# Kernel optimization log

Hardware: AMD Instinct MI355X
Metric: run time of the kernel (lower is better)

## Reference

```python
import jax, jax.numpy as jnp
import numpy as np

T, N, D, H, L = 256, 128, 1024, 1024, 2  # seq len, batch, input, hidden, layers


def setup_inputs() -> dict:
    key = jax.random.key(0)
    ks = jax.random.split(key, 7)
    s = 1.0 / np.sqrt(H)  # PyTorch LSTMCell init: U(-1/sqrt(H), 1/sqrt(H))
    return {
        "x": jax.random.normal(ks[0], (T, N, D), jnp.float32),
        "h0": jax.random.normal(ks[1], (L, N, H), jnp.float32),
        "c0": jax.random.normal(ks[2], (L, N, H), jnp.float32),
        # stacked per-layer params (layer 0 input dim == H so shapes match)
        "W_ih": jax.random.uniform(ks[3], (L, 4 * H, D), jnp.float32, -s, s),
        "W_hh": jax.random.uniform(ks[4], (L, 4 * H, H), jnp.float32, -s, s),
        "b_ih": jax.random.uniform(ks[5], (L, 4 * H), jnp.float32, -s, s),
        "b_hh": jax.random.uniform(ks[6], (L, 4 * H), jnp.float32, -s, s),
    }


def _lstm_cell(x, h, c, Wih, Whh, b):
    # gates layout (PyTorch order): input, forget, cell(g), output
    gates = x @ Wih.T + h @ Whh.T + b  # [N, 4H]
    i, f, g, o = jnp.split(gates, 4, axis=-1)
    c_new = jax.nn.sigmoid(f) * c + jax.nn.sigmoid(i) * jnp.tanh(g)
    h_new = jax.nn.sigmoid(o) * jnp.tanh(c_new)
    return h_new, c_new


def reference(x, h0, c0, W_ih, W_hh, b_ih, b_hh):
    num_layers = h0.shape[0]
    b = b_ih + b_hh  # [L, 4H]

    def step(carry, x_t):
        h, c = carry  # each [L, N, H]
        inp = x_t
        hs, cs = [], []
        for l in range(num_layers):  # small fixed layer count
            h_l, c_l = _lstm_cell(inp, h[l], c[l], W_ih[l], W_hh[l], b[l])
            hs.append(h_l)
            cs.append(c_l)
            inp = h_l  # mirrors x[t] = h[i] feeding the next layer
        return (jnp.stack(hs), jnp.stack(cs)), None

    (h, c), _ = jax.lax.scan(step, (h0, c0), x)
    return h[-1]  # [N, H] last layer hidden at final timestep
```

## Files before the change

kernel.cpp:

```cpp
#include <hip/hip_runtime.h>


typedef _Float16 f16;
typedef f16  v8f16 __attribute__((ext_vector_type(8)));
typedef float v4f32 __attribute__((ext_vector_type(4)));

#define TSTEPS 256
#define SLOT   131072u
static constexpr size_t HS_BANK = (size_t)258 * SLOT;

#define SZ_W     ((size_t)2*4096*2048*2)
#define SZ_B     ((size_t)2*4096*4)
#define SZ_HSEQ  ((size_t)2*258*SLOT*2)
#define SZ_BAR   ((size_t)8192)
#define SZ_XF    ((size_t)256*128*1024*2)
#define NEED1    (SZ_W + SZ_B + SZ_HSEQ + SZ_BAR)
#define NEED2    (NEED1 + SZ_XF)

__global__ void lstm_init(const float* __restrict__ x,
                          const float* __restrict__ h0,
                          const float* __restrict__ Wih, const float* __restrict__ Whh,
                          const float* __restrict__ bih, const float* __restrict__ bhh,
                          f16* __restrict__ wsW, float* __restrict__ wsB,
                          f16* __restrict__ hseq, unsigned* __restrict__ bar,
                          f16* __restrict__ xf, int do_xf)
{
    size_t tid  = (size_t)blockIdx.x * blockDim.x + threadIdx.x;
    size_t nthr = (size_t)gridDim.x * blockDim.x;
    for (size_t i = tid; i < 16777216u; i += nthr) {
        unsigned l = (unsigned)(i >> 23), rem = (unsigned)(i & 8388607u);
        unsigned col = rem >> 11, k = rem & 2047u;
        float v = (k < 1024u) ? Wih[(size_t)l*4194304u + (size_t)col*1024u + k]
                              : Whh[(size_t)l*4194304u + (size_t)col*1024u + (k-1024u)];
        wsW[i] = (f16)v;
    }
    for (size_t i = tid; i < 8192u; i += nthr) wsB[i] = bih[i] + bhh[i];
    for (size_t i = tid; i < 131072u; i += nthr) {
        unsigned n = (unsigned)(i >> 10), k = (unsigned)(i & 1023u);
        unsigned dst = ((k >> 3) << 10) + (n << 3) + (k & 7u);
        hseq[dst]           = (f16)h0[i];
        hseq[HS_BANK + dst] = (f16)h0[131072u + i];
    }
    for (size_t i = tid; i < 2048u; i += nthr) bar[i] = 0u;
    if (do_xf) {
        for (size_t i = tid; i < 33554432u; i += nthr) xf[i] = (f16)x[i];
    }
}

__device__ __forceinline__ float sigmoid_fast(float v) { return 1.0f / (1.0f + __expf(-v)); }
__device__ __forceinline__ float tanh_fast(float v)    { return 1.0f - 2.0f / (__expf(2.0f*v) + 1.0f); }

__device__ __forceinline__ v8f16 cvt8(v4f32 lo, v4f32 hi) {
    v8f16 r;
    r[0]=(f16)lo[0]; r[1]=(f16)lo[1]; r[2]=(f16)lo[2]; r[3]=(f16)lo[3];
    r[4]=(f16)hi[0]; r[5]=(f16)hi[1]; r[6]=(f16)hi[2]; r[7]=(f16)hi[3];
    return r;
}

__device__ __forceinline__ unsigned ld_cnt(const unsigned* p) {
    return __hip_atomic_load(p, __ATOMIC_RELAXED, __HIP_MEMORY_SCOPE_AGENT);
}

#define CHUNK 8

__device__ __forceinline__ void load_row(const f16* p, int off,
                                         v8f16 a0[CHUNK], v8f16 a1[CHUNK])
{
    #pragma unroll
    for (int i = 0; i < CHUNK; ++i) {
        a0[i] = *(const v8f16*)(p + off + 32*i);
        a1[i] = *(const v8f16*)(p + off + 16384 + 32*i);
    }
}

__device__ __forceinline__ void load_sm(const f16* p, int off,
                                        v8f16 a0[CHUNK], v8f16 a1[CHUNK])
{
    #pragma unroll
    for (int i = 0; i < CHUNK; ++i) {
        a0[i] = *(const v8f16*)(p + off + 4096*i);
        a1[i] = *(const v8f16*)(p + off + 128 + 4096*i);
    }
}

__device__ __forceinline__ void mfma_chunk(const v8f16 a0[CHUNK], const v8f16 a1[CHUNK],
                                           const f16 (*wl)[2056], int l15, int kq, int kbase,
                                           v4f32 acc[2][2])
{
    #pragma unroll
    for (int i = 0; i < CHUNK; ++i) {
        int k = kbase + 32*i;
        v8f16 b0 = *(const v8f16*)(&wl[l15     ][k + kq]);
        v8f16 b1 = *(const v8f16*)(&wl[16 + l15][k + kq]);
        acc[0][0] = __builtin_amdgcn_mfma_f32_16x16x32_f16(a0[i], b0, acc[0][0], 0, 0, 0);
        acc[0][1] = __builtin_amdgcn_mfma_f32_16x16x32_f16(a0[i], b1, acc[0][1], 0, 0, 0);
        acc[1][0] = __builtin_amdgcn_mfma_f32_16x16x32_f16(a1[i], b0, acc[1][0], 0, 0, 0);
        acc[1][1] = __builtin_amdgcn_mfma_f32_16x16x32_f16(a1[i], b1, acc[1][1], 0, 0, 0);
    }
}

__device__ __forceinline__ void reduce_splits(v4f32 acc[2][2], float (*gl)[36],
                                              int rb, int quad, int l15, int ks)
{
    if (ks == 0) {
        #pragma unroll
        for (int mt = 0; mt < 2; ++mt) {
            int rrow = (rb << 5) + (mt << 4) + (quad << 2);
            #pragma unroll
            for (int r = 0; r < 4; ++r) {
                gl[rrow + r][l15     ] = acc[mt][0][r];
                gl[rrow + r][16 + l15] = acc[mt][1][r];
            }
        }
    }
    __syncthreads();
    if (ks == 1) {
        #pragma unroll
        for (int mt = 0; mt < 2; ++mt) {
            int rrow = (rb << 5) + (mt << 4) + (quad << 2);
            #pragma unroll
            for (int r = 0; r < 4; ++r) {
                gl[rrow + r][l15     ] += acc[mt][0][r];
                gl[rrow + r][16 + l15] += acc[mt][1][r];
            }
        }
    }
    __syncthreads();
}

__device__ __forceinline__ void cell2(const float (*gl)[36], int n1, int u,
                                      float bi, float bf, float bg, float bo,
                                      float& cr0, float& cr1, float& h0o, float& h1o)
{
    {
        float gi = gl[n1][u]      + bi;
        float gf = gl[n1][8 + u]  + bf;
        float gg = gl[n1][16 + u] + bg;
        float go = gl[n1][24 + u] + bo;
        float cn = sigmoid_fast(gf) * cr0 + sigmoid_fast(gi) * tanh_fast(gg);
        cr0 = cn;
        h0o = sigmoid_fast(go) * tanh_fast(cn);
    }
    {
        int n = n1 + 64;
        float gi = gl[n][u]      + bi;
        float gf = gl[n][8 + u]  + bf;
        float gg = gl[n][16 + u] + bg;
        float go = gl[n][24 + u] + bo;
        float cn = sigmoid_fast(gf) * cr1 + sigmoid_fast(gi) * tanh_fast(gg);
        cr1 = cn;
        h1o = sigmoid_fast(go) * tanh_fast(cn);
    }
}

__device__ __forceinline__ void store_h_slot(f16 (*hst)[8], f16* slotbase, int s,
                                             int tid, int n1, int u,
                                             float hv0, float hv1)
{
    hst[n1     ][u] = (f16)hv0;
    hst[n1 + 64][u] = (f16)hv1;
    __syncthreads();
    if (tid < 128) {
        union { v8f16 v; unsigned long long q[2]; } c;
        c.v = *(const v8f16*)&hst[tid][0];
        unsigned long long* gp = (unsigned long long*)(slotbase + ((size_t)s << 10) + (tid << 3));
        __hip_atomic_store(gp,     c.q[0], __ATOMIC_RELAXED, __HIP_MEMORY_SCOPE_AGENT);
        __hip_atomic_store(gp + 1, c.q[1], __ATOMIC_RELAXED, __HIP_MEMORY_SCOPE_AGENT);
    }
}

template<bool XF16>
__global__ void __launch_bounds__(512)
lstm_main(const float* __restrict__ x, const f16* __restrict__ xf,
          const f16* __restrict__ wsW, const float* __restrict__ wsB,
          f16* __restrict__ hseq, const float* __restrict__ c0,
          float* __restrict__ out, unsigned* __restrict__ bar)
{
    __shared__ f16   wlds[32][2056];
    __shared__ float glds[128][36];
    __shared__ f16   hst[128][8];

    const int tid   = threadIdx.x;
    const int bid   = blockIdx.x;
    const int xcd   = bid & 7;
    const int layer = (xcd >> 2);
    const int s     = (bid >> 3) * 4 + (xcd & 3);
    const int lane  = tid & 63;
    const int wave  = tid >> 6;
    const int quad  = lane >> 4;
    const int l15   = lane & 15;
    const int rb    = wave & 3;
    const int ks    = wave >> 2;

    for (int idx = tid; idx < 8192; idx += 512) {
        int cc = idx >> 8;
        int k8 = (idx & 255) << 3;
        int col = ((cc >> 3) << 10) + (s << 3) + (cc & 7);
        *(v8f16*)(&wlds[cc][k8]) =
            *(const v8f16*)(wsW + (((size_t)(layer*4096 + col)) << 11) + k8);
    }

    const int u  = tid & 7;
    const int jg = (s << 3) + u;
    const float bi = wsB[layer*4096 +        jg];
    const float bf = wsB[layer*4096 + 1024 + jg];
    const float bg = wsB[layer*4096 + 2048 + jg];
    const float bo = wsB[layer*4096 + 3072 + jg];
    const int n1 = tid >> 3;
    float cr0 = c0[((size_t)layer << 17) + ((size_t)n1 << 10) + jg];
    float cr1 = c0[((size_t)layer << 17) + ((size_t)(n1 + 64) << 10) + jg];

    __syncthreads();

    const int kq   = quad << 3;
    const int row0 = (rb << 5) + l15;
    const int kslc = ks << 9;
    const int arow = (row0 << 10) + kslc + kq;
    const int jrow = (((kslc + kq) >> 3) << 10) + (row0 << 3);

    f16* h0b = hseq;
    f16* h1b = hseq + HS_BANK;
    unsigned* f0a = bar;
    unsigned* f0b = bar + 512;
    unsigned* f1  = bar + 1024;

    v8f16 A0[CHUNK], A1[CHUNK], C0[CHUNK], C1[CHUNK];

    if (layer == 0) {
        for (int t = 0; t < TSTEPS; ++t) {
            v4f32 acc[2][2] = {};

            if (XF16) {
                const f16* xp = xf + ((size_t)t << 17) + arow;
                load_row(xp, 0,   A0, A1);
                load_row(xp, 256, C0, C1);
                __builtin_amdgcn_sched_barrier(0);
                mfma_chunk(A0, A1, wlds, l15, kq, kslc,       acc);
                mfma_chunk(C0, C1, wlds, l15, kq, kslc + 256, acc);
            } else {
                const float* p0 = x + ((size_t)t << 17) + arow;
                const float* p1 = p0 + (16 << 10);
                #pragma unroll
                for (int k = 0; k < 512; k += 32) {
                    v4f32 w0 = *(const v4f32*)(p0 + k), w1 = *(const v4f32*)(p0 + k + 4);
                    v4f32 y0 = *(const v4f32*)(p1 + k), y1 = *(const v4f32*)(p1 + k + 4);
                    v8f16 a0 = cvt8(w0, w1);
                    v8f16 a1 = cvt8(y0, y1);
                    v8f16 b0 = *(const v8f16*)(&wlds[l15     ][kslc + k + kq]);
                    v8f16 b1 = *(const v8f16*)(&wlds[16 + l15][kslc + k + kq]);
                    acc[0][0] = __builtin_amdgcn_mfma_f32_16x16x32_f16(a0, b0, acc[0][0], 0, 0, 0);
                    acc[0][1] = __builtin_amdgcn_mfma_f32_16x16x32_f16(a0, b1, acc[0][1], 0, 0, 0);
                    acc[1][0] = __builtin_amdgcn_mfma_f32_16x16x32_f16(a1, b0, acc[1][0], 0, 0, 0);
                    acc[1][1] = __builtin_amdgcn_mfma_f32_16x16x32_f16(a1, b1, acc[1][1], 0, 0, 0);
                }
            }

            if (t > 0) {
                if (tid < 128) {
                    const unsigned* fp = f0a + (tid << 2);
                    unsigned need = (unsigned)t;
                    while (ld_cnt(fp) < need) __builtin_amdgcn_s_sleep(1);
                }
                __syncthreads();
            }

            {
                const f16* hp = h0b + (size_t)t * SLOT + jrow;
                load_sm(hp, 0,     A0, A1);
                load_sm(hp, 32768, C0, C1);
                __builtin_amdgcn_sched_barrier(0);
                mfma_chunk(A0, A1, wlds, l15, kq, 1024 + kslc,       acc);
                mfma_chunk(C0, C1, wlds, l15, kq, 1024 + kslc + 256, acc);
            }

            reduce_splits(acc, glds, rb, quad, l15, ks);

            float hv0, hv1;
            cell2(glds, n1, u, bi, bf, bg, bo, cr0, cr1, hv0, hv1);
            store_h_slot(hst, h0b + (size_t)(t + 1) * SLOT, s, tid, n1, u, hv0, hv1);

            __syncthreads();
            if (tid == 0) {
                __hip_atomic_store(f0a + (s << 2), (unsigned)(t + 1),
                                   __ATOMIC_RELAXED, __HIP_MEMORY_SCOPE_AGENT);
                __hip_atomic_store(f0b + (s << 2), (unsigned)(t + 1),
                                   __ATOMIC_RELAXED, __HIP_MEMORY_SCOPE_AGENT);
            }
        }
    } else {
        v8f16 D0[CHUNK], D1[CHUNK];
        for (int t = 0; t < TSTEPS; ++t) {
            {
                if (tid < 128) {
                    const unsigned* fp = f0b + (tid << 2);
                    unsigned need = (unsigned)(t + 1);
                    while (ld_cnt(fp) < need) __builtin_amdgcn_s_sleep(2);
                }
                __syncthreads();
            }

            v4f32 acc[2][2] = {};
            const f16* qp = h0b + (size_t)(t + 1) * SLOT + jrow;
            const f16* pp = h1b + (size_t)t * SLOT + jrow;

            load_sm(qp, 0,     A0, A1);
            load_sm(qp, 32768, C0, C1);
            __builtin_amdgcn_sched_barrier(0);

            if (t > 0) {
                if (tid < 128) {
                    const unsigned* fp = f1 + (tid << 2);
                    unsigned need = (unsigned)t;
                    while (ld_cnt(fp) < need) __builtin_amdgcn_s_sleep(2);
                }
            }
            __syncthreads();

            load_sm(pp, 0, D0, D1);
            __builtin_amdgcn_sched_barrier(0);
            mfma_chunk(A0, A1, wlds, l15, kq, kslc,       acc);
            load_sm(pp, 32768, A0, A1);
            __builtin_amdgcn_sched_barrier(0);
            mfma_chunk(C0, C1, wlds, l15, kq, kslc + 256, acc);
            mfma_chunk(D0, D1, wlds, l15, kq, 1024 + kslc,       acc);
            mfma_chunk(A0, A1, wlds, l15, kq, 1024 + kslc + 256, acc);

            reduce_splits(acc, glds, rb, quad, l15, ks);

            float hv0, hv1;
            cell2(glds, n1, u, bi, bf, bg, bo, cr0, cr1, hv0, hv1);
            if (t < TSTEPS - 1) {
                store_h_slot(hst, h1b + (size_t)(t + 1) * SLOT, s, tid, n1, u, hv0, hv1);
                __syncthreads();
                if (tid == 0)
                    __hip_atomic_store(f1 + (s << 2), (unsigned)(t + 1),
                                       __ATOMIC_RELAXED, __HIP_MEMORY_SCOPE_AGENT);
            } else {
                out[(n1 << 10) + jg] = hv0;
                out[((n1 + 64) << 10) + jg] = hv1;
            }
        }
    }
}

extern "C" void kernel_launch(void* const* d_in, const int* in_sizes, int n_in,
                              void* d_out, int out_size, void* d_ws, size_t ws_size,
                              hipStream_t stream) {
    const float* x   = (const float*)d_in[0];
    const float* h0  = (const float*)d_in[1];
    const float* c0  = (const float*)d_in[2];
    const float* Wih = (const float*)d_in[3];
    const float* Whh = (const float*)d_in[4];
    const float* bih = (const float*)d_in[5];
    const float* bhh = (const float*)d_in[6];
    float* out = (float*)d_out;

    char* ws = (char*)d_ws;
    const bool xf16 = (ws_size >= NEED2);

    f16*      wsW  = (f16*)ws;
    float*    wsB  = (float*)(ws + SZ_W);
    f16*      hseq = (f16*)(ws + SZ_W + SZ_B);
    unsigned* bar  = (unsigned*)(ws + SZ_W + SZ_B + SZ_HSEQ);
    f16*      xf   = (f16*)(ws + NEED1);
    int do_xf = xf16 ? 1 : 0;

    lstm_init<<<2048, 256, 0, stream>>>(x, h0, Wih, Whh, bih, bhh,
                                        wsW, wsB, hseq, bar, xf, do_xf);

    void* kargs[] = { (void*)&x, (void*)&xf, (void*)&wsW, (void*)&wsB,
                      (void*)&hseq, (void*)&c0, (void*)&out, (void*)&bar };
    if (xf16) {
        hipLaunchCooperativeKernel((void*)&lstm_main<true>, dim3(256), dim3(512), kargs, 0, stream);
    } else {
        hipLaunchCooperativeKernel((void*)&lstm_main<false>, dim3(256), dim3(512), kargs, 0, stream);
    }
}
```

Baseline: 3.139 ms.

## Precompute layer-0 input projections for all timesteps in a parallel prologue

Adds a prologue in which all 256 blocks (both layer groups, using layer-0 weights) compute x_t @ W_ih0^T for every timestep and write the gate preactivations to a workspace buffer in fp32 or fp16. A grid-wide flag barrier follows, then layer-1 blocks reload their own weights. The recurrent layer-0 loop then only does the h @ W_hh part and adds a prefetched gx vector, which shortens the serial critical path. This costs an extra large workspace buffer plus its memory traffic and a global barrier. Which variant runs depends on how much workspace is available.

After: 3.631 ms. 1.16x slower.

```diff
diff --git a/kernel.cpp b/kernel.cpp
--- a/kernel.cpp
+++ b/kernel.cpp
@@ -12,10 +12,14 @@
 #define SZ_W     ((size_t)2*4096*2048*2)
 #define SZ_B     ((size_t)2*4096*4)
 #define SZ_HSEQ  ((size_t)2*258*SLOT*2)
-#define SZ_BAR   ((size_t)8192)
+#define SZ_BAR   ((size_t)16384)
 #define SZ_XF    ((size_t)256*128*1024*2)
 #define NEED1    (SZ_W + SZ_B + SZ_HSEQ + SZ_BAR)
 #define NEED2    (NEED1 + SZ_XF)
+#define SZ_GX32  ((size_t)256*128*4096*4)
+#define SZ_GX16  ((size_t)256*128*4096*2)
+#define NEED3_32 (NEED2 + SZ_GX32)
+#define NEED3_16 (NEED2 + SZ_GX16)
 
 __global__ void lstm_init(const float* __restrict__ x,
                           const float* __restrict__ h0,
@@ -41,7 +45,7 @@
         hseq[dst]           = (f16)h0[i];
         hseq[HS_BANK + dst] = (f16)h0[131072u + i];
     }
-    for (size_t i = tid; i < 2048u; i += nthr) bar[i] = 0u;
+    for (size_t i = tid; i < 4096u; i += nthr) bar[i] = 0u;
     if (do_xf) {
         for (size_t i = tid; i < 33554432u; i += nthr) xf[i] = (f16)x[i];
     }
@@ -129,24 +133,25 @@
 }
 
 __device__ __forceinline__ void cell2(const float (*gl)[36], int n1, int u,
+                                      const float* gxv,
                                       float bi, float bf, float bg, float bo,
                                       float& cr0, float& cr1, float& h0o, float& h1o)
 {
     {
-        float gi = gl[n1][u]      + bi;
-        float gf = gl[n1][8 + u]  + bf;
-        float gg = gl[n1][16 + u] + bg;
-        float go = gl[n1][24 + u] + bo;
+        float gi = gl[n1][u]      + gxv[0] + bi;
+        float gf = gl[n1][8 + u]  + gxv[1] + bf;
+        float gg = gl[n1][16 + u] + gxv[2] + bg;
+        float go = gl[n1][24 + u] + gxv[3] + bo;
         float cn = sigmoid_fast(gf) * cr0 + sigmoid_fast(gi) * tanh_fast(gg);
         cr0 = cn;
         h0o = sigmoid_fast(go) * tanh_fast(cn);
     }
     {
         int n = n1 + 64;
-        float gi = gl[n][u]      + bi;
-        float gf = gl[n][8 + u]  + bf;
-        float gg = gl[n][16 + u] + bg;
-        float go = gl[n][24 + u] + bo;
+        float gi = gl[n][u]      + gxv[4] + bi;
+        float gf = gl[n][8 + u]  + gxv[5] + bf;
+        float gg = gl[n][16 + u] + gxv[6] + bg;
+        float go = gl[n][24 + u] + gxv[7] + bo;
         float cn = sigmoid_fast(gf) * cr1 + sigmoid_fast(gi) * tanh_fast(gg);
         cr1 = cn;
         h1o = sigmoid_fast(go) * tanh_fast(cn);
@@ -169,12 +174,41 @@
     }
 }
 
-template<bool XF16>
+__device__ __forceinline__ void stage_w(f16 (*wl)[2056], const f16* wsW,
+                                        int lyr, int s, int tid)
+{
+    for (int idx = tid; idx < 8192; idx += 512) {
+        int cc = idx >> 8;
+        int k8 = (idx & 255) << 3;
+        int col = ((cc >> 3) << 10) + (s << 3) + (cc & 7);
+        *(v8f16*)(&wl[cc][k8]) =
+            *(const v8f16*)(wsW + (((size_t)(lyr*4096 + col)) << 11) + k8);
+    }
+}
+
+template<int MODE>
+__device__ __forceinline__ void load_gx(const void* gxws, int t, int s, int tid, float gxv[8])
+{
+    size_t ge = (((size_t)t << 7) + (size_t)s) * 4096u + ((size_t)tid << 3);
+    if constexpr (MODE == 2) {
+        const v4f32* gp = (const v4f32*)((const float*)gxws + ge);
+        v4f32 ga = gp[0], gb = gp[1];
+        gxv[0]=ga[0]; gxv[1]=ga[1]; gxv[2]=ga[2]; gxv[3]=ga[3];
+        gxv[4]=gb[0]; gxv[5]=gb[1]; gxv[6]=gb[2]; gxv[7]=gb[3];
+    } else {
+        v8f16 gv = *(const v8f16*)((const f16*)gxws + ge);
+        #pragma unroll
+        for (int i = 0; i < 8; ++i) gxv[i] = (float)gv[i];
+    }
+}
+
+template<int MODE, bool XF16>
 __global__ void __launch_bounds__(512)
 lstm_main(const float* __restrict__ x, const f16* __restrict__ xf,
           const f16* __restrict__ wsW, const float* __restrict__ wsB,
           f16* __restrict__ hseq, const float* __restrict__ c0,
-          float* __restrict__ out, unsigned* __restrict__ bar)
+          float* __restrict__ out, unsigned* __restrict__ bar,
+          void* gxws)
 {
     __shared__ f16   wlds[32][2056];
     __shared__ float glds[128][36];
@@ -192,13 +226,7 @@
     const int rb    = wave & 3;
     const int ks    = wave >> 2;
 
-    for (int idx = tid; idx < 8192; idx += 512) {
-        int cc = idx >> 8;
-        int k8 = (idx & 255) << 3;
-        int col = ((cc >> 3) << 10) + (s << 3) + (cc & 7);
-        *(v8f16*)(&wlds[cc][k8]) =
-            *(const v8f16*)(wsW + (((size_t)(layer*4096 + col)) << 11) + k8);
-    }
+    stage_w(wlds, wsW, (MODE >= 1 && layer == 1) ? 0 : layer, s, tid);
 
     const int u  = tid & 7;
     const int jg = (s << 3) + u;
@@ -220,38 +248,94 @@
 
     f16* h0b = hseq;
     f16* h1b = hseq + HS_BANK;
-    unsigned* f0a = bar;
-    unsigned* f0b = bar + 512;
-    unsigned* f1  = bar + 1024;
+    unsigned* f0a  = bar;
+    unsigned* f0b  = bar + 512;
+    unsigned* f1   = bar + 1024;
+    unsigned* prep = bar + 1536;
 
     v8f16 A0[CHUNK], A1[CHUNK], C0[CHUNK], C1[CHUNK];
+    float gz[8] = {0,0,0,0,0,0,0,0};
+
+    if constexpr (MODE >= 1) {
+        const int tbase = (layer == 0) ? 0 : 128;
+        for (int tt = 0; tt < 128; ++tt) {
+            const int t = tbase + tt;
+            v4f32 acc[2][2] = {};
+            const f16* xp = xf + ((size_t)t << 17) + arow;
+            load_row(xp, 0,   A0, A1);
+            load_row(xp, 256, C0, C1);
+            __builtin_amdgcn_sched_barrier(0);
+            mfma_chunk(A0, A1, wlds, l15, kq, kslc,       acc);
+            mfma_chunk(C0, C1, wlds, l15, kq, kslc + 256, acc);
+            reduce_splits(acc, glds, rb, quad, l15, ks);
+            float g0 = glds[n1][u],      g1 = glds[n1][8+u];
+            float g2 = glds[n1][16+u],   g3 = glds[n1][24+u];
+            float g4 = glds[n1+64][u],   g5 = glds[n1+64][8+u];
+            float g6 = glds[n1+64][16+u],g7 = glds[n1+64][24+u];
+            __syncthreads();
+            size_t ge = (((size_t)t << 7) + (size_t)s) * 4096u + ((size_t)tid << 3);
+            if constexpr (MODE == 2) {
+                union { float f[8]; unsigned long long q[4]; } gu;
+                gu.f[0]=g0; gu.f[1]=g1; gu.f[2]=g2; gu.f[3]=g3;
+                gu.f[4]=g4; gu.f[5]=g5; gu.f[6]=g6; gu.f[7]=g7;
+                unsigned long long* gp = (unsigned long long*)((float*)gxws + ge);
+                #pragma unroll
+                for (int i = 0; i < 4; ++i)
+                    __hip_atomic_store(gp + i, gu.q[i],
+                                       __ATOMIC_RELAXED, __HIP_MEMORY_SCOPE_AGENT);
+            } else {
+                union { f16 h[8]; unsigned long long q[2]; } gh;
+                gh.h[0]=(f16)g0; gh.h[1]=(f16)g1; gh.h[2]=(f16)g2; gh.h[3]=(f16)g3;
+                gh.h[4]=(f16)g4; gh.h[5]=(f16)g5; gh.h[6]=(f16)g6; gh.h[7]=(f16)g7;
+                unsigned long long* gp = (unsigned long long*)((f16*)gxws + ge);
+                __hip_atomic_store(gp,     gh.q[0], __ATOMIC_RELAXED, __HIP_MEMORY_SCOPE_AGENT);
+                __hip_atomic_store(gp + 1, gh.q[1], __ATOMIC_RELAXED, __HIP_MEMORY_SCOPE_AGENT);
+            }
+        }
+        __syncthreads();
+        if (tid == 0)
+            __hip_atomic_store(prep + (((layer << 7) | s) << 2), 1u,
+                               __ATOMIC_RELAXED, __HIP_MEMORY_SCOPE_AGENT);
+        if (tid < 256) {
+            const unsigned* fp = prep + (tid << 2);
+            while (ld_cnt(fp) < 1u) __builtin_amdgcn_s_sleep(2);
+        }
+        __syncthreads();
+        if (layer == 1) stage_w(wlds, wsW, 1, s, tid);
+        __syncthreads();
+    }
 
     if (layer == 0) {
+        float gxv[8];
+        if constexpr (MODE >= 1) load_gx<MODE>(gxws, 0, s, tid, gxv);
+
         for (int t = 0; t < TSTEPS; ++t) {
             v4f32 acc[2][2] = {};
 
-            if (XF16) {
-                const f16* xp = xf + ((size_t)t << 17) + arow;
-                load_row(xp, 0,   A0, A1);
-                load_row(xp, 256, C0, C1);
-                __builtin_amdgcn_sched_barrier(0);
-                mfma_chunk(A0, A1, wlds, l15, kq, kslc,       acc);
-                mfma_chunk(C0, C1, wlds, l15, kq, kslc + 256, acc);
-            } else {
-                const float* p0 = x + ((size_t)t << 17) + arow;
-                const float* p1 = p0 + (16 << 10);
-                #pragma unroll
-                for (int k = 0; k < 512; k += 32) {
-                    v4f32 w0 = *(const v4f32*)(p0 + k), w1 = *(const v4f32*)(p0 + k + 4);
-                    v4f32 y0 = *(const v4f32*)(p1 + k), y1 = *(const v4f32*)(p1 + k + 4);
-                    v8f16 a0 = cvt8(w0, w1);
-                    v8f16 a1 = cvt8(y0, y1);
-                    v8f16 b0 = *(const v8f16*)(&wlds[l15     ][kslc + k + kq]);
-                    v8f16 b1 = *(const v8f16*)(&wlds[16 + l15][kslc + k + kq]);
-                    acc[0][0] = __builtin_amdgcn_mfma_f32_16x16x32_f16(a0, b0, acc[0][0], 0, 0, 0);
-                    acc[0][1] = __builtin_amdgcn_mfma_f32_16x16x32_f16(a0, b1, acc[0][1], 0, 0, 0);
-                    acc[1][0] = __builtin_amdgcn_mfma_f32_16x16x32_f16(a1, b0, acc[1][0], 0, 0, 0);
-                    acc[1][1] = __builtin_amdgcn_mfma_f32_16x16x32_f16(a1, b1, acc[1][1], 0, 0, 0);
+            if constexpr (MODE == 0) {
+                if (XF16) {
+                    const f16* xp = xf + ((size_t)t << 17) + arow;
+                    load_row(xp, 0,   A0, A1);
+                    load_row(xp, 256, C0, C1);
+                    __builtin_amdgcn_sched_barrier(0);
+                    mfma_chunk(A0, A1, wlds, l15, kq, kslc,       acc);
+                    mfma_chunk(C0, C1, wlds, l15, kq, kslc + 256, acc);
+                } else {
+                    const float* p0 = x + ((size_t)t << 17) + arow;
+                    const float* p1 = p0 + (16 << 10);
+                    #pragma unroll
+                    for (int k = 0; k < 512; k += 32) {
+                        v4f32 w0 = *(const v4f32*)(p0 + k), w1 = *(const v4f32*)(p0 + k + 4);
+                        v4f32 y0 = *(const v4f32*)(p1 + k), y1 = *(const v4f32*)(p1 + k + 4);
+                        v8f16 a0 = cvt8(w0, w1);
+                        v8f16 a1 = cvt8(y0, y1);
+                        v8f16 b0 = *(const v8f16*)(&wlds[l15     ][kslc + k + kq]);
+                        v8f16 b1 = *(const v8f16*)(&wlds[16 + l15][kslc + k + kq]);
+                        acc[0][0] = __builtin_amdgcn_mfma_f32_16x16x32_f16(a0, b0, acc[0][0], 0, 0, 0);
+                        acc[0][1] = __builtin_amdgcn_mfma_f32_16x16x32_f16(a0, b1, acc[0][1], 0, 0, 0);
+                        acc[1][0] = __builtin_amdgcn_mfma_f32_16x16x32_f16(a1, b0, acc[1][0], 0, 0, 0);
+                        acc[1][1] = __builtin_amdgcn_mfma_f32_16x16x32_f16(a1, b1, acc[1][1], 0, 0, 0);
+                    }
                 }
             }
 
@@ -276,7 +360,7 @@
             reduce_splits(acc, glds, rb, quad, l15, ks);
 
             float hv0, hv1;
-            cell2(glds, n1, u, bi, bf, bg, bo, cr0, cr1, hv0, hv1);
+            cell2(glds, n1, u, (MODE >= 1) ? gxv : gz, bi, bf, bg, bo, cr0, cr1, hv0, hv1);
             store_h_slot(hst, h0b + (size_t)(t + 1) * SLOT, s, tid, n1, u, hv0, hv1);
 
             __syncthreads();
@@ -285,6 +369,9 @@
                                    __ATOMIC_RELAXED, __HIP_MEMORY_SCOPE_AGENT);
                 __hip_atomic_store(f0b + (s << 2), (unsigned)(t + 1),
                                    __ATOMIC_RELAXED, __HIP_MEMORY_SCOPE_AGENT);
+            }
+            if constexpr (MODE >= 1) {
+                if (t + 1 < TSTEPS) load_gx<MODE>(gxws, t + 1, s, tid, gxv);
             }
         }
     } else {
@@ -328,7 +415,7 @@
             reduce_splits(acc, glds, rb, quad, l15, ks);
 
             float hv0, hv1;
-            cell2(glds, n1, u, bi, bf, bg, bo, cr0, cr1, hv0, hv1);
+            cell2(glds, n1, u, gz, bi, bf, bg, bo, cr0, cr1, hv0, hv1);
             if (t < TSTEPS - 1) {
                 store_h_slot(hst, h1b + (size_t)(t + 1) * SLOT, s, tid, n1, u, hv0, hv1);
                 __syncthreads();
@@ -363,16 +450,22 @@
     f16*      hseq = (f16*)(ws + SZ_W + SZ_B);
     unsigned* bar  = (unsigned*)(ws + SZ_W + SZ_B + SZ_HSEQ);
     f16*      xf   = (f16*)(ws + NEED1);
+    void*     gxws = (void*)(ws + NEED2);
     int do_xf = xf16 ? 1 : 0;
 
     lstm_init<<<2048, 256, 0, stream>>>(x, h0, Wih, Whh, bih, bhh,
                                         wsW, wsB, hseq, bar, xf, do_xf);
 
     void* kargs[] = { (void*)&x, (void*)&xf, (void*)&wsW, (void*)&wsB,
-                      (void*)&hseq, (void*)&c0, (void*)&out, (void*)&bar };
-    if (xf16) {
-        hipLaunchCooperativeKernel((void*)&lstm_main<true>, dim3(256), dim3(512), kargs, 0, stream);
+                      (void*)&hseq, (void*)&c0, (void*)&out, (void*)&bar,
+                      (void*)&gxws };
+    if (ws_size >= NEED3_32) {
+        hipLaunchCooperativeKernel((void*)&lstm_main<2, true>, dim3(256), dim3(512), kargs, 0, stream);
+    } else if (ws_size >= NEED3_16) {
+        hipLaunchCooperativeKernel((void*)&lstm_main<1, true>, dim3(256), dim3(512), kargs, 0, stream);
+    } else if (xf16) {
+        hipLaunchCooperativeKernel((void*)&lstm_main<0, true>, dim3(256), dim3(512), kargs, 0, stream);
     } else {
-        hipLaunchCooperativeKernel((void*)&lstm_main<false>, dim3(256), dim3(512), kargs, 0, stream);
-    }
-}
+        hipLaunchCooperativeKernel((void*)&lstm_main<0, false>, dim3(256), dim3(512), kargs, 0, stream);
+    }
+}
```
